# Performance work log

Measured on AMD Instinct MI355X. Metric: run time of the kernel, lower is better.

## Reference

```python
import jax, jax.numpy as jnp
import numpy as np

B, S, D = 4, 2048, 1024
H, HD = 16, 64
ROT_DIM = 64
ROT_BASE = 10000.0


def setup_inputs() -> dict:
    key = jax.random.key(0)
    ks = jax.random.split(key, 5)
    return {
        "hidden_states": jax.random.normal(ks[0], (B, S, D), dtype=jnp.float32),
        "Wqkv_w": jax.random.normal(ks[1], (3 * D, D), dtype=jnp.float32) * 0.02,
        "Wqkv_b": jax.random.normal(ks[2], (3 * D,), dtype=jnp.float32) * 0.02,
        "Wo_w": jax.random.normal(ks[3], (D, D), dtype=jnp.float32) * 0.02,
        "Wo_b": jax.random.normal(ks[4], (D,), dtype=jnp.float32) * 0.02,
    }


def _rope_cos_sin(seqlen, dtype):
    inv_freq = 1.0 / (ROT_BASE ** (jnp.arange(0, ROT_DIM, 2, dtype=jnp.float32) / ROT_DIM))
    t = jnp.arange(seqlen, dtype=jnp.float32)
    freqs = jnp.einsum("s,f->sf", t, inv_freq)  # (S, ROT_DIM//2)
    return jnp.cos(freqs).astype(dtype), jnp.sin(freqs).astype(dtype)


def _apply_rope(x, cos, sin):
    # x: (B, S, H, HD), non-interleaved rotary on first ROT_DIM dims
    ro, pas = x[..., :ROT_DIM], x[..., ROT_DIM:]
    x1, x2 = ro[..., : ROT_DIM // 2], ro[..., ROT_DIM // 2 :]
    c = cos[None, :, None, :]  # (1, S, 1, ROT_DIM//2)
    s = sin[None, :, None, :]
    rot = jnp.concatenate([x1 * c - x2 * s, x1 * s + x2 * c], axis=-1)
    return jnp.concatenate([rot, pas], axis=-1) if pas.shape[-1] else rot


def reference(hidden_states, Wqkv_w, Wqkv_b, Wo_w, Wo_b):
    b, s, d = hidden_states.shape
    qkv = hidden_states @ Wqkv_w.T + Wqkv_b  # (B, S, 3D)
    qkv = qkv.reshape(b, s, 3, H, HD)
    q, k, v = qkv[:, :, 0], qkv[:, :, 1], qkv[:, :, 2]  # each (B, S, H, HD)
    cos, sin = _rope_cos_sin(s, hidden_states.dtype)
    q = _apply_rope(q, cos, sin)
    k = _apply_rope(k, cos, sin)
    scale = 1.0 / jnp.sqrt(jnp.asarray(HD, hidden_states.dtype))
    scores = jnp.einsum("bqhd,bkhd->bhqk", q, k) * scale
    probs = jax.nn.softmax(scores, axis=-1)
    attn = jnp.einsum("bhqk,bkhd->bqhd", probs, v)  # (B, S, H, HD)
    attn = attn.reshape(b, s, d)
    return attn @ Wo_w.T + Wo_b
```

## Files before the change

### kernel.cpp

```cpp
#include <hip/hip_runtime.h>
#include <hip/hip_bf16.h>
#include <cstdint>
#include <cstddef>

typedef __bf16 bf16;
typedef __bf16 bf16x4 __attribute__((ext_vector_type(4)));
typedef __bf16 bf16x8 __attribute__((ext_vector_type(8)));
typedef float f32x4 __attribute__((ext_vector_type(4)));

#define NB 4
#define NS 2048
#define ND 1024
#define NH 16
#define NHD 64
#define NM (NB * NS)

#define QSCALE 0.18033688011112042f

__device__ inline void lds_dma16(const bf16* g, bf16* l) {
    __builtin_amdgcn_global_load_lds(
        (const __attribute__((address_space(1))) void*)g,
        (__attribute__((address_space(3))) void*)l, 16, 0, 0);
}

#define NHS4 2097152
#define NWQ4 786432
#define NWO4 262144
__global__ void prep_kernel(const float4* __restrict__ hs, const float4* __restrict__ wq,
                            const float4* __restrict__ wo,
                            float* __restrict__ cost, float* __restrict__ sint,
                            bf16x4* __restrict__ X, bf16x4* __restrict__ Wb,
                            bf16x4* __restrict__ Wob) {
    int i = blockIdx.x * 256 + threadIdx.x;
    if (i < NS * 32) {
        int s = i >> 5, f = i & 31;
        float inv = exp2f(-(float)f * (13.287712379549449f / 32.0f));
        float ang = (float)s * inv;
        cost[i] = cosf(ang);
        sint[i] = sinf(ang);
    }
    if (i < NHS4) {
        float4 v = hs[i];
        bf16x4 r = {(bf16)v.x, (bf16)v.y, (bf16)v.z, (bf16)v.w};
        X[i] = r;
    } else if (i < NHS4 + NWQ4) {
        int j = i - NHS4;
        float4 v = wq[j];
        bf16x4 r = {(bf16)v.x, (bf16)v.y, (bf16)v.z, (bf16)v.w};
        Wb[j] = r;
    } else {
        int j = i - NHS4 - NWQ4;
        float4 v = wo[j];
        bf16x4 r = {(bf16)v.x, (bf16)v.y, (bf16)v.z, (bf16)v.w};
        Wob[j] = r;
    }
}

__global__ void cvt_bf16_kernel(const float4* __restrict__ in, bf16x4* __restrict__ out) {
    int i = blockIdx.x * 256 + threadIdx.x;
    float4 v = in[i];
    bf16x4 r = {(bf16)v.x, (bf16)v.y, (bf16)v.z, (bf16)v.w};
    out[i] = r;
}

__global__ void __launch_bounds__(256) qkv_rope_gemm(
    const bf16* __restrict__ A, const bf16* __restrict__ W,
    const float* __restrict__ bias,
    const float* __restrict__ cost, const float* __restrict__ sint,
    bf16* __restrict__ Qw, bf16* __restrict__ Kw, bf16* __restrict__ Vt) {
    __shared__ __attribute__((aligned(16))) bf16 lA[2][128 * 32];
    __shared__ __attribute__((aligned(16))) bf16 lB[2][128 * 32];

    int t = threadIdx.x, lane = t & 63, w = t >> 6;
    int col = lane & 15, quad = lane >> 4;
    int p = blockIdx.y * 24 + blockIdx.x;
    int L = (p & 7) * 192 + (p >> 3);
    int bx = L % 24, by = L / 24;
    int m0 = by * 128, n0 = bx * 128;
    int wm = (w >> 1) * 64, wn = (w & 1) * 64;

    f32x4 acc[4][4];
#pragma unroll
    for (int i = 0; i < 4; ++i)
#pragma unroll
        for (int j = 0; j < 4; ++j) acc[i][j] = (f32x4){0.f, 0.f, 0.f, 0.f};

    const bf16* gA0 = A + (size_t)(m0 + w * 32 + (lane >> 2)) * ND + (lane & 3) * 8;
    const bf16* gA1 = gA0 + (size_t)16 * ND;
    const bf16* gB0 = W + (size_t)(n0 + w * 32 + (lane >> 2)) * ND + (lane & 3) * 8;
    const bf16* gB1 = gB0 + (size_t)16 * ND;
    bf16* la = &lA[0][0];
    bf16* lb = &lB[0][0];
    int sA0 = w * 1024, sA1 = w * 1024 + 512;

    lds_dma16(gA0, la + sA0);
    lds_dma16(gA1, la + sA1);
    lds_dma16(gB0, lb + sA0);
    lds_dma16(gB1, lb + sA1);
    asm volatile("s_waitcnt vmcnt(0)" ::: "memory");
    __builtin_amdgcn_s_barrier();
    asm volatile("" ::: "memory");

#pragma unroll 2
    for (int kt = 0; kt < 32; ++kt) {
        int cur = kt & 1, nb = cur ^ 1;
        if (kt + 1 < 32) {
            int kn = (kt + 1) * 32;
            lds_dma16(gA0 + kn, la + nb * 4096 + sA0);
            lds_dma16(gA1 + kn, la + nb * 4096 + sA1);
            lds_dma16(gB0 + kn, lb + nb * 4096 + sA0);
            lds_dma16(gB1 + kn, lb + nb * 4096 + sA1);
        }
        const bf16* lac = la + cur * 4096;
        const bf16* lbc = lb + cur * 4096;
        bf16x8 af[4], bg[4];
#pragma unroll
        for (int i = 0; i < 4; ++i)
            af[i] = *(const bf16x8*)&lac[(wm + i * 16 + col) * 32 + quad * 8];
#pragma unroll
        for (int j = 0; j < 4; ++j)
            bg[j] = *(const bf16x8*)&lbc[(wn + j * 16 + col) * 32 + quad * 8];
        __builtin_amdgcn_s_setprio(1);
#pragma unroll
        for (int i = 0; i < 4; ++i)
#pragma unroll
            for (int j = 0; j < 4; ++j)
                acc[i][j] = __builtin_amdgcn_mfma_f32_16x16x32_bf16(af[i], bg[j], acc[i][j], 0, 0, 0);
        __builtin_amdgcn_s_setprio(0);
        if (kt + 1 < 32) asm volatile("s_waitcnt vmcnt(0)" ::: "memory");
        __builtin_amdgcn_s_barrier();
        asm volatile("" ::: "memory");
    }

    int nseg = n0 + wn;
    int which = nseg >> 10;
    int h = (nseg >> 6) & (NH - 1);
    float bj[4];
#pragma unroll
    for (int j = 0; j < 4; ++j) bj[j] = bias[nseg + j * 16 + col];

    if (which == 2) {
        int mbase = m0 + wm;
        int b = mbase >> 11;
        bf16* dsth = Vt + (size_t)(b * NH + h) * NHD * NS;
#pragma unroll
        for (int i = 0; i < 4; ++i) {
            int s = ((mbase + i * 16) & (NS - 1)) + quad * 4;
#pragma unroll
            for (int j = 0; j < 4; ++j) {
                bf16x4 pv = {(bf16)(acc[i][j][0] + bj[j]), (bf16)(acc[i][j][1] + bj[j]),
                             (bf16)(acc[i][j][2] + bj[j]), (bf16)(acc[i][j][3] + bj[j])};
                *(bf16x4*)(dsth + (size_t)(j * 16 + col) * NS + s) = pv;
            }
        }
    } else {
        float sc = which ? 1.0f : QSCALE;
#pragma unroll
        for (int i = 0; i < 4; ++i) {
#pragma unroll
            for (int r = 0; r < 4; ++r) {
                int m = m0 + wm + i * 16 + quad * 4 + r;
                int b = m >> 11, s = m & (NS - 1);
                float v0 = acc[i][0][r] + bj[0];
                float v1 = acc[i][1][r] + bj[1];
                float v2 = acc[i][2][r] + bj[2];
                float v3 = acc[i][3][r] + bj[3];
                bf16* dst = (which ? Kw : Qw) + ((size_t)(b * NH + h) * NS + s) * NHD;
                float c0 = cost[s * 32 + col], s0 = sint[s * 32 + col];
                float c1 = cost[s * 32 + 16 + col], s1 = sint[s * 32 + 16 + col];
                dst[col] = (bf16)((v0 * c0 - v2 * s0) * sc);
                dst[16 + col] = (bf16)((v1 * c1 - v3 * s1) * sc);
                dst[32 + col] = (bf16)((v0 * s0 + v2 * c0) * sc);
                dst[48 + col] = (bf16)((v1 * s1 + v3 * c1) * sc);
            }
        }
    }
}

__global__ void __launch_bounds__(256, 2) attn_kernel(
    const bf16* __restrict__ Qw, const bf16* __restrict__ Kw,
    const bf16* __restrict__ Vt, bf16* __restrict__ X) {
    const int LDK = 72;
    const int LV = 36;
    __shared__ __attribute__((aligned(16))) bf16 lK[2][32 * LDK];
    __shared__ __attribute__((aligned(16))) bf16 lV[2][64 * LV];

    int t = threadIdx.x, lane = t & 63, w = t >> 6;
    int col = lane & 15, q = lane >> 4;
    int bh = blockIdx.y, b = bh >> 4, h = bh & 15;
    int q0 = blockIdx.x * 256 + w * 64;
    const bf16* Qh = Qw + (size_t)bh * NS * NHD;
    const bf16* Kh = Kw + (size_t)bh * NS * NHD;
    const bf16* Vh = Vt + (size_t)bh * NHD * NS;

    int krow = t >> 3, kc = t & 7;
    int vrow = t >> 2, vc = t & 3;
    const bf16* gK = Kh + (size_t)krow * NHD + kc * 8;
    const bf16* gV = Vh + (size_t)vrow * NS + vc * 8;
    int wKoff = krow * LDK + kc * 8;
    int wVoff = vrow * LV + vc * 8;

    bf16x8 bQ[4][2];
#pragma unroll
    for (int mb = 0; mb < 4; ++mb)
#pragma unroll
        for (int h2 = 0; h2 < 2; ++h2)
            bQ[mb][h2] = *(const bf16x8*)(Qh + (size_t)(q0 + mb * 16 + col) * NHD + h2 * 32 + q * 8);

    f32x4 o[4][4];
#pragma unroll
    for (int mb = 0; mb < 4; ++mb)
#pragma unroll
        for (int hb = 0; hb < 4; ++hb) o[mb][hb] = (f32x4){0.f, 0.f, 0.f, 0.f};
    f32x4 dacc[4];
#pragma unroll
    for (int mb = 0; mb < 4; ++mb) dacc[mb] = (f32x4){0.f, 0.f, 0.f, 0.f};

    const bf16 one = (bf16)1.0f;
    bf16x8 ones = {one, one, one, one, one, one, one, one};

    bf16x8 kr[2], vr[2];
    kr[0] = *(const bf16x8*)gK;
    vr[0] = *(const bf16x8*)gV;
    kr[1] = *(const bf16x8*)(gK + (size_t)32 * NHD);
    vr[1] = *(const bf16x8*)(gV + 32);
    *(bf16x8*)&lK[0][wKoff] = kr[0];
    *(bf16x8*)&lV[0][wVoff] = vr[0];

#pragma unroll 2
    for (int it = 0; it < 64; ++it) {
        __syncthreads();
        int cur = it & 1, nxt = cur ^ 1;
        if (it + 2 < 64) {
            kr[cur] = *(const bf16x8*)(gK + (size_t)(it + 2) * 32 * NHD);
            vr[cur] = *(const bf16x8*)(gV + (it + 2) * 32);
        }

        bf16x8 aK[2][2];
#pragma unroll
        for (int tb = 0; tb < 2; ++tb)
#pragma unroll
            for (int h2 = 0; h2 < 2; ++h2)
                aK[tb][h2] = *(const bf16x8*)&lK[cur][(tb * 16 + col) * LDK + h2 * 32 + q * 8];
        bf16x8 vf[4];
#pragma unroll
        for (int hb = 0; hb < 4; ++hb) {
            const bf16* vp = &lV[cur][(hb * 16 + col) * LV + q * 4];
            bf16x4 lo = *(const bf16x4*)vp;
            bf16x4 hi = *(const bf16x4*)(vp + 16);
            vf[hb] = __builtin_shufflevector(lo, hi, 0, 1, 2, 3, 4, 5, 6, 7);
        }
        __builtin_amdgcn_s_setprio(1);
#pragma unroll
        for (int mb = 0; mb < 4; ++mb) {
            f32x4 s0 = (f32x4){0.f, 0.f, 0.f, 0.f};
            f32x4 s1 = (f32x4){0.f, 0.f, 0.f, 0.f};
            s0 = __builtin_amdgcn_mfma_f32_16x16x32_bf16(aK[0][0], bQ[mb][0], s0, 0, 0, 0);
            s0 = __builtin_amdgcn_mfma_f32_16x16x32_bf16(aK[0][1], bQ[mb][1], s0, 0, 0, 0);
            s1 = __builtin_amdgcn_mfma_f32_16x16x32_bf16(aK[1][0], bQ[mb][0], s1, 0, 0, 0);
            s1 = __builtin_amdgcn_mfma_f32_16x16x32_bf16(aK[1][1], bQ[mb][1], s1, 0, 0, 0);
            bf16x8 pf;
#pragma unroll
            for (int r = 0; r < 4; ++r) {
                float p0 = __builtin_amdgcn_exp2f(s0[r]);
                float p1 = __builtin_amdgcn_exp2f(s1[r]);
                pf[r] = (bf16)p0;
                pf[4 + r] = (bf16)p1;
            }
            dacc[mb] = __builtin_amdgcn_mfma_f32_16x16x32_bf16(ones, pf, dacc[mb], 0, 0, 0);
#pragma unroll
            for (int hb = 0; hb < 4; ++hb)
                o[mb][hb] = __builtin_amdgcn_mfma_f32_16x16x32_bf16(vf[hb], pf, o[mb][hb], 0, 0, 0);
        }
        __builtin_amdgcn_s_setprio(0);

        if (it + 1 < 64) {
            *(bf16x8*)&lK[nxt][wKoff] = kr[nxt];
            *(bf16x8*)&lV[nxt][wVoff] = vr[nxt];
        }
    }

#pragma unroll
    for (int mb = 0; mb < 4; ++mb) {
        float linv = 1.0f / dacc[mb][0];
        int s = q0 + mb * 16 + col;
        bf16* dst = X + (size_t)(b * NS + s) * ND + h * NHD;
#pragma unroll
        for (int hb = 0; hb < 4; ++hb) {
            bf16x4 ov = {(bf16)(o[mb][hb][0] * linv), (bf16)(o[mb][hb][1] * linv),
                         (bf16)(o[mb][hb][2] * linv), (bf16)(o[mb][hb][3] * linv)};
            *(bf16x4*)(dst + hb * 16 + q * 4) = ov;
        }
    }
}

__global__ void __launch_bounds__(256) out_gemm(
    const bf16* __restrict__ A, const bf16* __restrict__ W,
    const float* __restrict__ bias, float* __restrict__ out) {
    __shared__ __attribute__((aligned(16))) bf16 lA[2][128 * 32];
    __shared__ __attribute__((aligned(16))) bf16 lB[2][128 * 32];

    int t = threadIdx.x, lane = t & 63, w = t >> 6;
    int col = lane & 15, quad = lane >> 4;
    int p = blockIdx.y * 8 + blockIdx.x;
    int L = (p & 7) * 64 + (p >> 3);
    int bx = L & 7, by = L >> 3;
    int m0 = by * 128, n0 = bx * 128;
    int wm = (w >> 1) * 64, wn = (w & 1) * 64;

    f32x4 acc[4][4];
#pragma unroll
    for (int i = 0; i < 4; ++i)
#pragma unroll
        for (int j = 0; j < 4; ++j) acc[i][j] = (f32x4){0.f, 0.f, 0.f, 0.f};

    const bf16* gA0 = A + (size_t)(m0 + w * 32 + (lane >> 2)) * ND + (lane & 3) * 8;
    const bf16* gA1 = gA0 + (size_t)16 * ND;
    const bf16* gB0 = W + (size_t)(n0 + w * 32 + (lane >> 2)) * ND + (lane & 3) * 8;
    const bf16* gB1 = gB0 + (size_t)16 * ND;
    bf16* la = &lA[0][0];
    bf16* lb = &lB[0][0];
    int sA0 = w * 1024, sA1 = w * 1024 + 512;

    lds_dma16(gA0, la + sA0);
    lds_dma16(gA1, la + sA1);
    lds_dma16(gB0, lb + sA0);
    lds_dma16(gB1, lb + sA1);
    asm volatile("s_waitcnt vmcnt(0)" ::: "memory");
    __builtin_amdgcn_s_barrier();
    asm volatile("" ::: "memory");

#pragma unroll 2
    for (int kt = 0; kt < 32; ++kt) {
        int cur = kt & 1, nb = cur ^ 1;
        if (kt + 1 < 32) {
            int kn = (kt + 1) * 32;
            lds_dma16(gA0 + kn, la + nb * 4096 + sA0);
            lds_dma16(gA1 + kn, la + nb * 4096 + sA1);
            lds_dma16(gB0 + kn, lb + nb * 4096 + sA0);
            lds_dma16(gB1 + kn, lb + nb * 4096 + sA1);
        }
        const bf16* lac = la + cur * 4096;
        const bf16* lbc = lb + cur * 4096;
        bf16x8 af[4], bg[4];
#pragma unroll
        for (int i = 0; i < 4; ++i)
            af[i] = *(const bf16x8*)&lac[(wm + i * 16 + col) * 32 + quad * 8];
#pragma unroll
        for (int j = 0; j < 4; ++j)
            bg[j] = *(const bf16x8*)&lbc[(wn + j * 16 + col) * 32 + quad * 8];
        __builtin_amdgcn_s_setprio(1);
#pragma unroll
        for (int i = 0; i < 4; ++i)
#pragma unroll
            for (int j = 0; j < 4; ++j)
                acc[i][j] = __builtin_amdgcn_mfma_f32_16x16x32_bf16(af[i], bg[j], acc[i][j], 0, 0, 0);
        __builtin_amdgcn_s_setprio(0);
        if (kt + 1 < 32) asm volatile("s_waitcnt vmcnt(0)" ::: "memory");
        __builtin_amdgcn_s_barrier();
        asm volatile("" ::: "memory");
    }

    float bj[4];
#pragma unroll
    for (int j = 0; j < 4; ++j) bj[j] = bias[n0 + wn + j * 16 + col];
#pragma unroll
    for (int i = 0; i < 4; ++i)
#pragma unroll
        for (int r = 0; r < 4; ++r) {
            int m = m0 + wm + i * 16 + quad * 4 + r;
#pragma unroll
            for (int j = 0; j < 4; ++j)
                out[(size_t)m * ND + n0 + wn + j * 16 + col] = acc[i][j][r] + bj[j];
        }
}

extern "C" void kernel_launch(void* const* d_in, const int* in_sizes, int n_in,
                              void* d_out, int out_size, void* d_ws, size_t ws_size,
                              hipStream_t stream) {
    const float* hs = (const float*)d_in[0];
    const float* Wqkv = (const float*)d_in[1];
    const float* bqkv = (const float*)d_in[2];
    const float* Wo = (const float*)d_in[3];
    const float* bo = (const float*)d_in[4];
    float* out = (float*)d_out;

    char* ws = (char*)d_ws;
    float* cost = (float*)ws;
    float* sint = cost + NS * 32;
    bf16* Qw = (bf16*)(ws + 524288);
    bf16* Kw = Qw + (size_t)NB * NH * NS * NHD;
    bf16* Vt = Kw + (size_t)NB * NH * NS * NHD;
    bf16* X = Vt + (size_t)NB * NH * NS * NHD;
    bf16* Wqkv_b = (bf16*)d_out;

    const size_t base_end = 524288 + (size_t)4 * NB * NH * NS * NHD * 2;
    bool fuse_wo = ws_size >= base_end + (size_t)ND * ND * 2;
    bf16* Wo_b = fuse_wo ? (bf16*)(ws + base_end) : Qw;

    int prep_blocks = (NHS4 + NWQ4 + (fuse_wo ? NWO4 : 0)) / 256;
    prep_kernel<<<dim3(prep_blocks), dim3(256), 0, stream>>>(
        (const float4*)hs, (const float4*)Wqkv, (const float4*)Wo,
        cost, sint, (bf16x4*)X, (bf16x4*)Wqkv_b, (bf16x4*)Wo_b);
    qkv_rope_gemm<<<dim3(3 * ND / 128, NM / 128), dim3(256), 0, stream>>>(
        X, Wqkv_b, bqkv, cost, sint, Qw, Kw, Vt);
    attn_kernel<<<dim3(NS / 256, NB * NH), dim3(256), 0, stream>>>(Qw, Kw, Vt, X);
    if (!fuse_wo)
        cvt_bf16_kernel<<<dim3(ND * ND / 4 / 256), dim3(256), 0, stream>>>(
            (const float4*)Wo, (bf16x4*)Wo_b);
    out_gemm<<<dim3(ND / 128, NM / 128), dim3(256), 0, stream>>>(X, Wo_b, bo, out);
}
```

Measured before the change: 265.5 us.

## Triple-buffer LDS in QKV and output GEMMs, drop swizzled block mapping

Both projection GEMMs move from double to triple-buffered LDS. The next-next K tile is prefetched and the loop waits with vmcnt(4), so one tile's loads stay in flight across the barrier. This is meant to hide more global-load latency behind the MFMA work. It also removes the grouped block-index remapping in favour of plain blockIdx tiling, which may hurt L2 reuse, and the larger LDS footprint per block may lower occupancy.

Result: slower. 285.0 us (+7.4%).

```diff
diff --git a/kernel.cpp b/kernel.cpp
--- a/kernel.cpp
+++ b/kernel.cpp
@@ -68,15 +68,12 @@
     const float* __restrict__ bias,
     const float* __restrict__ cost, const float* __restrict__ sint,
     bf16* __restrict__ Qw, bf16* __restrict__ Kw, bf16* __restrict__ Vt) {
-    __shared__ __attribute__((aligned(16))) bf16 lA[2][128 * 32];
-    __shared__ __attribute__((aligned(16))) bf16 lB[2][128 * 32];
+    __shared__ __attribute__((aligned(16))) bf16 lA[3][128 * 32];
+    __shared__ __attribute__((aligned(16))) bf16 lB[3][128 * 32];
 
     int t = threadIdx.x, lane = t & 63, w = t >> 6;
     int col = lane & 15, quad = lane >> 4;
-    int p = blockIdx.y * 24 + blockIdx.x;
-    int L = (p & 7) * 192 + (p >> 3);
-    int bx = L % 24, by = L / 24;
-    int m0 = by * 128, n0 = bx * 128;
+    int m0 = blockIdx.y * 128, n0 = blockIdx.x * 128;
     int wm = (w >> 1) * 64, wn = (w & 1) * 64;
 
     f32x4 acc[4][4];
@@ -89,30 +86,33 @@
     const bf16* gA1 = gA0 + (size_t)16 * ND;
     const bf16* gB0 = W + (size_t)(n0 + w * 32 + (lane >> 2)) * ND + (lane & 3) * 8;
     const bf16* gB1 = gB0 + (size_t)16 * ND;
-    bf16* la = &lA[0][0];
-    bf16* lb = &lB[0][0];
-    int sA0 = w * 1024, sA1 = w * 1024 + 512;
-
-    lds_dma16(gA0, la + sA0);
-    lds_dma16(gA1, la + sA1);
-    lds_dma16(gB0, lb + sA0);
-    lds_dma16(gB1, lb + sA1);
-    asm volatile("s_waitcnt vmcnt(0)" ::: "memory");
+    int sOff = w * 1024;
+
+    lds_dma16(gA0, &lA[0][sOff]);
+    lds_dma16(gA1, &lA[0][sOff + 512]);
+    lds_dma16(gB0, &lB[0][sOff]);
+    lds_dma16(gB1, &lB[0][sOff + 512]);
+    lds_dma16(gA0 + 32, &lA[1][sOff]);
+    lds_dma16(gA1 + 32, &lA[1][sOff + 512]);
+    lds_dma16(gB0 + 32, &lB[1][sOff]);
+    lds_dma16(gB1 + 32, &lB[1][sOff + 512]);
+    asm volatile("s_waitcnt vmcnt(4)" ::: "memory");
     __builtin_amdgcn_s_barrier();
     asm volatile("" ::: "memory");
 
-#pragma unroll 2
+    int cur = 0;
     for (int kt = 0; kt < 32; ++kt) {
-        int cur = kt & 1, nb = cur ^ 1;
-        if (kt + 1 < 32) {
-            int kn = (kt + 1) * 32;
-            lds_dma16(gA0 + kn, la + nb * 4096 + sA0);
-            lds_dma16(gA1 + kn, la + nb * 4096 + sA1);
-            lds_dma16(gB0 + kn, lb + nb * 4096 + sA0);
-            lds_dma16(gB1 + kn, lb + nb * 4096 + sA1);
-        }
-        const bf16* lac = la + cur * 4096;
-        const bf16* lbc = lb + cur * 4096;
+        int nb2 = cur + 2;
+        if (nb2 >= 3) nb2 -= 3;
+        if (kt + 2 < 32) {
+            int kn = (kt + 2) * 32;
+            lds_dma16(gA0 + kn, &lA[nb2][sOff]);
+            lds_dma16(gA1 + kn, &lA[nb2][sOff + 512]);
+            lds_dma16(gB0 + kn, &lB[nb2][sOff]);
+            lds_dma16(gB1 + kn, &lB[nb2][sOff + 512]);
+        }
+        const bf16* lac = &lA[cur][0];
+        const bf16* lbc = &lB[cur][0];
         bf16x8 af[4], bg[4];
 #pragma unroll
         for (int i = 0; i < 4; ++i)
@@ -127,9 +127,16 @@
             for (int j = 0; j < 4; ++j)
                 acc[i][j] = __builtin_amdgcn_mfma_f32_16x16x32_bf16(af[i], bg[j], acc[i][j], 0, 0, 0);
         __builtin_amdgcn_s_setprio(0);
-        if (kt + 1 < 32) asm volatile("s_waitcnt vmcnt(0)" ::: "memory");
-        __builtin_amdgcn_s_barrier();
-        asm volatile("" ::: "memory");
+        if (kt + 2 < 32) {
+            asm volatile("s_waitcnt vmcnt(4)" ::: "memory");
+            __builtin_amdgcn_s_barrier();
+            asm volatile("" ::: "memory");
+        } else if (kt + 1 < 32) {
+            asm volatile("s_waitcnt vmcnt(0)" ::: "memory");
+            __builtin_amdgcn_s_barrier();
+            asm volatile("" ::: "memory");
+        }
+        cur = (cur + 1 == 3) ? 0 : cur + 1;
     }
 
     int nseg = n0 + wn;
@@ -297,15 +304,12 @@
 __global__ void __launch_bounds__(256) out_gemm(
     const bf16* __restrict__ A, const bf16* __restrict__ W,
     const float* __restrict__ bias, float* __restrict__ out) {
-    __shared__ __attribute__((aligned(16))) bf16 lA[2][128 * 32];
-    __shared__ __attribute__((aligned(16))) bf16 lB[2][128 * 32];
+    __shared__ __attribute__((aligned(16))) bf16 lA[3][128 * 32];
+    __shared__ __attribute__((aligned(16))) bf16 lB[3][128 * 32];
 
     int t = threadIdx.x, lane = t & 63, w = t >> 6;
     int col = lane & 15, quad = lane >> 4;
-    int p = blockIdx.y * 8 + blockIdx.x;
-    int L = (p & 7) * 64 + (p >> 3);
-    int bx = L & 7, by = L >> 3;
-    int m0 = by * 128, n0 = bx * 128;
+    int m0 = blockIdx.y * 128, n0 = blockIdx.x * 128;
     int wm = (w >> 1) * 64, wn = (w & 1) * 64;
 
     f32x4 acc[4][4];
@@ -318,30 +322,33 @@
     const bf16* gA1 = gA0 + (size_t)16 * ND;
     const bf16* gB0 = W + (size_t)(n0 + w * 32 + (lane >> 2)) * ND + (lane & 3) * 8;
     const bf16* gB1 = gB0 + (size_t)16 * ND;
-    bf16* la = &lA[0][0];
-    bf16* lb = &lB[0][0];
-    int sA0 = w * 1024, sA1 = w * 1024 + 512;
-
-    lds_dma16(gA0, la + sA0);
-    lds_dma16(gA1, la + sA1);
-    lds_dma16(gB0, lb + sA0);
-    lds_dma16(gB1, lb + sA1);
-    asm volatile("s_waitcnt vmcnt(0)" ::: "memory");
+    int sOff = w * 1024;
+
+    lds_dma16(gA0, &lA[0][sOff]);
+    lds_dma16(gA1, &lA[0][sOff + 512]);
+    lds_dma16(gB0, &lB[0][sOff]);
+    lds_dma16(gB1, &lB[0][sOff + 512]);
+    lds_dma16(gA0 + 32, &lA[1][sOff]);
+    lds_dma16(gA1 + 32, &lA[1][sOff + 512]);
+    lds_dma16(gB0 + 32, &lB[1][sOff]);
+    lds_dma16(gB1 + 32, &lB[1][sOff + 512]);
+    asm volatile("s_waitcnt vmcnt(4)" ::: "memory");
     __builtin_amdgcn_s_barrier();
     asm volatile("" ::: "memory");
 
-#pragma unroll 2
+    int cur = 0;
     for (int kt = 0; kt < 32; ++kt) {
-        int cur = kt & 1, nb = cur ^ 1;
-        if (kt + 1 < 32) {
-            int kn = (kt + 1) * 32;
-            lds_dma16(gA0 + kn, la + nb * 4096 + sA0);
-            lds_dma16(gA1 + kn, la + nb * 4096 + sA1);
-            lds_dma16(gB0 + kn, lb + nb * 4096 + sA0);
-            lds_dma16(gB1 + kn, lb + nb * 4096 + sA1);
-        }
-        const bf16* lac = la + cur * 4096;
-        const bf16* lbc = lb + cur * 4096;
+        int nb2 = cur + 2;
+        if (nb2 >= 3) nb2 -= 3;
+        if (kt + 2 < 32) {
+            int kn = (kt + 2) * 32;
+            lds_dma16(gA0 + kn, &lA[nb2][sOff]);
+            lds_dma16(gA1 + kn, &lA[nb2][sOff + 512]);
+            lds_dma16(gB0 + kn, &lB[nb2][sOff]);
+            lds_dma16(gB1 + kn, &lB[nb2][sOff + 512]);
+        }
+        const bf16* lac = &lA[cur][0];
+        const bf16* lbc = &lB[cur][0];
         bf16x8 af[4], bg[4];
 #pragma unroll
         for (int i = 0; i < 4; ++i)
@@ -356,9 +363,16 @@
             for (int j = 0; j < 4; ++j)
                 acc[i][j] = __builtin_amdgcn_mfma_f32_16x16x32_bf16(af[i], bg[j], acc[i][j], 0, 0, 0);
         __builtin_amdgcn_s_setprio(0);
-        if (kt + 1 < 32) asm volatile("s_waitcnt vmcnt(0)" ::: "memory");
-        __builtin_amdgcn_s_barrier();
-        asm volatile("" ::: "memory");
+        if (kt + 2 < 32) {
+            asm volatile("s_waitcnt vmcnt(4)" ::: "memory");
+            __builtin_amdgcn_s_barrier();
+            asm volatile("" ::: "memory");
+        } else if (kt + 1 < 32) {
+            asm volatile("s_waitcnt vmcnt(0)" ::: "memory");
+            __builtin_amdgcn_s_barrier();
+            asm volatile("" ::: "memory");
+        }
+        cur = (cur + 1 == 3) ? 0 : cur + 1;
     }
 
     float bj[4];
```
